# Optimization experiments

Hardware: AMD Instinct MI355X
Metric: run time of the kernel (lower is better)

Reference implementation:

```python
import jax, jax.numpy as jnp
import numpy as np

B, IN, D = 4096, 2048, 2048
NAMES = ["inpgate", "rec_inpgate", "mem_inpgate", "inp", "rec_inp", "readgate",
         "rec_readgate", "mem_readgate", "decoder", "writegate", "rec_writegate",
         "mem_writegate", "encoder"]


def setup_inputs() -> dict:
    key = jax.random.key(0)
    ks = jax.random.split(key, 1 + len(NAMES))
    inp = {
        "x": jax.random.normal(ks[0], (B, IN), jnp.float32),
        "out0": jnp.zeros((B, D), jnp.float32),   # recurrent output state (reset())
        "mem0": jnp.zeros((B, D), jnp.float32),   # memory state (reset())
    }
    for i, n in enumerate(NAMES):
        inp["w_" + n] = jax.random.normal(ks[1 + i], (D, D), jnp.float32) * 0.02
        inp["b_" + n] = jnp.zeros((D,), jnp.float32)
    return inp


def _lin(v, W, b):
    # torch nn.Linear: y = v @ W.T + b, W is [out, in]
    return v @ W.T + b


def reference(x, out0, mem0,
              w_inpgate, b_inpgate, w_rec_inpgate, b_rec_inpgate,
              w_mem_inpgate, b_mem_inpgate, w_inp, b_inp,
              w_rec_inp, b_rec_inp, w_readgate, b_readgate,
              w_rec_readgate, b_rec_readgate, w_mem_readgate, b_mem_readgate,
              w_decoder, b_decoder, w_writegate, b_writegate,
              w_rec_writegate, b_rec_writegate, w_mem_writegate, b_mem_writegate,
              w_encoder, b_encoder):
    sig = jax.nn.sigmoid
    # input block (note: original uses sigmoid here, not tanh)
    block_inp = sig(_lin(x, w_inp, b_inp) + _lin(out0, w_rec_inp, b_rec_inp))
    inp_gate = sig(_lin(x, w_inpgate, b_inpgate)
                   + _lin(mem0, w_mem_inpgate, b_mem_inpgate)
                   + _lin(out0, w_rec_inpgate, b_rec_inpgate))
    read_gate = sig(_lin(x, w_readgate, b_readgate)
                    + _lin(mem0, w_mem_readgate, b_mem_readgate)
                    + _lin(out0, w_rec_readgate, b_rec_readgate))
    decoded_mem = _lin(read_gate * mem0, w_decoder, b_decoder)
    hidden = decoded_mem + block_inp * inp_gate
    write_gate = sig(_lin(x, w_writegate, b_writegate)
                     + _lin(mem0, w_mem_writegate, b_mem_writegate)
                     + _lin(out0, w_rec_writegate, b_rec_writegate))
    enc = jnp.tanh(_lin(hidden, w_encoder, b_encoder))
    mem = (1.0 - write_gate) * mem0 + write_gate * enc
    # torch forward() returns self.out (== hidden_act); mem is internal state
    return hidden
```

## Files before the change

### kernel.cpp

```cpp
#include <hip/hip_runtime.h>
#include <stdint.h>


typedef short bf16x8 __attribute__((ext_vector_type(8)));
typedef float f32x4 __attribute__((ext_vector_type(4)));

#define AS1(p) ((__attribute__((address_space(1))) void*)(uintptr_t)(p))
#define AS3(p) ((__attribute__((address_space(3))) void*)(uint32_t)(uintptr_t)(p))
#define GLD16(gp, lp) __builtin_amdgcn_global_load_lds(AS1(gp), AS3(lp), 16, 0, 0)

__device__ __forceinline__ unsigned short f2bf(float f) {
  union { float f; unsigned u; } c; c.f = f;
  unsigned u = c.u;
  unsigned r = (u + 0x7FFFu + ((u >> 16) & 1u)) >> 16;
  return (unsigned short)r;
}
__device__ __forceinline__ float bf2f(unsigned short h) {
  union { unsigned u; float f; } c; c.u = ((unsigned)h) << 16;
  return c.f;
}
__device__ __forceinline__ float sigf(float x) {
  return 1.0f / (1.0f + __expf(-x));
}

__global__ void init_flags_kernel(int* flags) {
  if (threadIdx.x < 2) flags[threadIdx.x] = 0;
}

struct ConvActArgs {
  const float4* src[3];
  ushort4* dst[3];
  int flagidx[3];
  int n4;
  int* flags;
};

__global__ void conv_acts_kernel(ConvActArgs a) {
  const int arr = blockIdx.y;
  const float4* __restrict__ s = a.src[arr];
  ushort4* __restrict__ d = a.dst[arr];
  unsigned nz = 0;
  for (int i = blockIdx.x * blockDim.x + threadIdx.x; i < a.n4;
       i += gridDim.x * blockDim.x) {
    float4 v = s[i];
    union { float f; unsigned u; } cx, cy, cz, cw;
    cx.f = v.x; cy.f = v.y; cz.f = v.z; cw.f = v.w;
    nz |= cx.u | cy.u | cz.u | cw.u;
    ushort4 o;
    o.x = f2bf(v.x); o.y = f2bf(v.y); o.z = f2bf(v.z); o.w = f2bf(v.w);
    d[i] = o;
  }
  const int fi = a.flagidx[arr];
  if (fi >= 0) {
    if (__any(nz != 0u) && (threadIdx.x & 63) == 0) atomicOr(&a.flags[fi], 1);
  }
}

struct ConvWArgs {
  const float4* src[9];
  ushort4* dst[9];
  int flagidx[9];
  int n4;
  const int* flags;
};

__global__ void conv_weights_kernel(ConvWArgs a) {
  const int arr = blockIdx.y;
  const int fi = a.flagidx[arr];
  if (fi >= 0 && a.flags[fi] == 0) return;
  const float4* __restrict__ s = a.src[arr];
  ushort4* __restrict__ d = a.dst[arr];
  for (int i = blockIdx.x * blockDim.x + threadIdx.x; i < a.n4;
       i += gridDim.x * blockDim.x) {
    float4 v = s[i];
    ushort4 o;
    o.x = f2bf(v.x); o.y = f2bf(v.y); o.z = f2bf(v.z); o.w = f2bf(v.w);
    d[i] = o;
  }
}

struct Job {
  const unsigned short* A0; const unsigned short* W0; const float* b0;
  const unsigned short* A1; const unsigned short* W1; const float* b1;
  const unsigned short* A2; const unsigned short* W2; const float* b2;
  int f0, f1, f2;
  int npairs;
  int jobf;
  const int* flags;
  const float* add;
  float* outF;
  unsigned short* outH;
};

__global__ void __launch_bounds__(256)
gemm_bt_multi(Job j0, Job j1, Job j2) {
  __shared__ __attribute__((aligned(16))) unsigned short sA[128 * 64];
  __shared__ __attribute__((aligned(16))) unsigned short sB[128 * 64];

  const Job jb = (blockIdx.z == 0) ? j0 : ((blockIdx.z == 1) ? j1 : j2);
  if (jb.jobf >= 0 && jb.flags[jb.jobf] == 0) return;

  const int tid = threadIdx.x;
  const int l = tid & 63;
  const int w = tid >> 6;
  const int wm = w >> 1, wn = w & 1;
  const int bm = blockIdx.y, bn = blockIdx.x;

  f32x4 acc[4][4];
#pragma unroll
  for (int i = 0; i < 4; ++i)
#pragma unroll
    for (int j = 0; j < 4; ++j) acc[i][j] = (f32x4){0.f, 0.f, 0.f, 0.f};

  const int srow = l >> 3;
  const int kchS = (l & 7) ^ srow;
  const long long laneA = ((long long)bm * 128 + srow) * 2048 + kchS * 8;
  const long long laneB = ((long long)bn * 128 + srow) * 2048 + kchS * 8;

  auto do_pair = [&](const unsigned short* Ap, const unsigned short* Wp) {
    const unsigned short* ga = Ap + laneA;
    const unsigned short* gb = Wp + laneB;
    for (int kt = 0; kt < 32; ++kt) {
#pragma unroll
      for (int ii = 0; ii < 4; ++ii) {
        const int q = w * 4 + ii;
        GLD16(ga + (long long)(q * 8) * 2048, (char*)sA + q * 1024);
        GLD16(gb + (long long)(q * 8) * 2048, (char*)sB + q * 1024);
      }
      __syncthreads();

#pragma unroll
      for (int ks = 0; ks < 2; ++ks) {
        bf16x8 af[4], bf[4];
        const int c = ks * 4 + (l >> 4);
#pragma unroll
        for (int i = 0; i < 4; ++i) {
          const int ra = wm * 64 + i * 16 + (l & 15);
          const int rb = wn * 64 + i * 16 + (l & 15);
          af[i] = *(const bf16x8*)((const char*)sA +
                  (ra * 128 + ((c ^ (ra & 7)) * 16)));
          bf[i] = *(const bf16x8*)((const char*)sB +
                  (rb * 128 + ((c ^ (rb & 7)) * 16)));
        }
#pragma unroll
        for (int i = 0; i < 4; ++i)
#pragma unroll
          for (int j = 0; j < 4; ++j)
            acc[i][j] = __builtin_amdgcn_mfma_f32_16x16x32_bf16(
                af[i], bf[j], acc[i][j], 0, 0, 0);
      }
      __syncthreads();
      ga += 64;
      gb += 64;
    }
  };

  if (jb.f0 < 0 || jb.flags[jb.f0]) do_pair(jb.A0, jb.W0);
  if (jb.npairs > 1 && (jb.f1 < 0 || jb.flags[jb.f1])) do_pair(jb.A1, jb.W1);
  if (jb.npairs > 2 && (jb.f2 < 0 || jb.flags[jb.f2])) do_pair(jb.A2, jb.W2);

  const int colb = bn * 128 + wn * 64;
  const int rowb = bm * 128 + wm * 64;
#pragma unroll
  for (int j = 0; j < 4; ++j) {
    const int col = colb + j * 16 + (l & 15);
    float bias = 0.f;
    if (jb.b0) bias += jb.b0[col];
    if (jb.npairs > 1 && jb.b1) bias += jb.b1[col];
    if (jb.npairs > 2 && jb.b2) bias += jb.b2[col];
#pragma unroll
    for (int i = 0; i < 4; ++i) {
      const int row0 = rowb + i * 16 + (l >> 4) * 4;
#pragma unroll
      for (int r = 0; r < 4; ++r) {
        const long long idx = (long long)(row0 + r) * 2048 + col;
        float v = acc[i][j][r] + bias;
        if (jb.add) v += jb.add[idx];
        if (jb.outF) jb.outF[idx] = v;
        else jb.outH[idx] = f2bf(v);
      }
    }
  }
}

__global__ void gates_kernel(const ushort4* __restrict__ u1,
                             const ushort4* __restrict__ u2,
                             const ushort4* __restrict__ u3,
                             const float4* __restrict__ mem0,
                             float4* __restrict__ g, ushort4* __restrict__ rg,
                             int n4) {
  int i = blockIdx.x * blockDim.x + threadIdx.x;
  if (i >= n4) return;
  ushort4 a = u1[i], b = u2[i], c = u3[i];
  float4 m = mem0[i];
  float4 go;
  ushort4 ro;
  go.x = sigf(bf2f(a.x)) * sigf(bf2f(b.x)); ro.x = f2bf(sigf(bf2f(c.x)) * m.x);
  go.y = sigf(bf2f(a.y)) * sigf(bf2f(b.y)); ro.y = f2bf(sigf(bf2f(c.y)) * m.y);
  go.z = sigf(bf2f(a.z)) * sigf(bf2f(b.z)); ro.z = f2bf(sigf(bf2f(c.z)) * m.z);
  go.w = sigf(bf2f(a.w)) * sigf(bf2f(b.w)); ro.w = f2bf(sigf(bf2f(c.w)) * m.w);
  g[i] = go;
  rg[i] = ro;
}

extern "C" void kernel_launch(void* const* d_in, const int* in_sizes, int n_in,
                              void* d_out, int out_size, void* d_ws, size_t ws_size,
                              hipStream_t stream) {
  (void)in_sizes; (void)n_in; (void)out_size; (void)ws_size;
  const int Bx = 4096, Dx = 2048;
  const size_t ACT = (size_t)Bx * Dx;
  const size_t WEL = (size_t)Dx * Dx;

  const float* x    = (const float*)d_in[0];
  const float* out0 = (const float*)d_in[1];
  const float* mem0 = (const float*)d_in[2];
  const float* w_inpgate     = (const float*)d_in[3];
  const float* b_inpgate     = (const float*)d_in[4];
  const float* w_rec_inpgate = (const float*)d_in[5];
  const float* b_rec_inpgate = (const float*)d_in[6];
  const float* w_mem_inpgate = (const float*)d_in[7];
  const float* b_mem_inpgate = (const float*)d_in[8];
  const float* w_inp         = (const float*)d_in[9];
  const float* b_inp         = (const float*)d_in[10];
  const float* w_rec_inp     = (const float*)d_in[11];
  const float* b_rec_inp     = (const float*)d_in[12];
  const float* w_readgate    = (const float*)d_in[13];
  const float* b_readgate    = (const float*)d_in[14];
  const float* w_rec_readgate= (const float*)d_in[15];
  const float* b_rec_readgate= (const float*)d_in[16];
  const float* w_mem_readgate= (const float*)d_in[17];
  const float* b_mem_readgate= (const float*)d_in[18];
  const float* w_decoder     = (const float*)d_in[19];
  const float* b_decoder     = (const float*)d_in[20];

  char* ws = (char*)d_ws;
  unsigned short* xb  = (unsigned short*)(ws);
  unsigned short* o0b = xb + ACT;
  unsigned short* m0b = o0b + ACT;
  unsigned short* wb  = m0b + ACT;
  unsigned short* u1 = wb + 9 * WEL;
  unsigned short* u2 = u1 + ACT;
  unsigned short* u3 = u2 + ACT;
  float* g = (float*)(u3 + ACT);
  unsigned short* rg = (unsigned short*)(g + ACT);
  int* flags = (int*)(rg + ACT);

  init_flags_kernel<<<1, 64, 0, stream>>>(flags);

  ConvActArgs aa;
  aa.src[0] = (const float4*)x;    aa.dst[0] = (ushort4*)xb;  aa.flagidx[0] = -1;
  aa.src[1] = (const float4*)out0; aa.dst[1] = (ushort4*)o0b; aa.flagidx[1] = 0;
  aa.src[2] = (const float4*)mem0; aa.dst[2] = (ushort4*)m0b; aa.flagidx[2] = 1;
  aa.n4 = (int)(ACT / 4);
  aa.flags = flags;
  conv_acts_kernel<<<dim3(2048, 3, 1), 256, 0, stream>>>(aa);

  ConvWArgs wa;
  const float* wsrc[9] = {w_inp, w_rec_inp, w_inpgate, w_mem_inpgate,
                          w_rec_inpgate, w_readgate, w_mem_readgate,
                          w_rec_readgate, w_decoder};
  const int wflag[9] = {-1, 0, -1, 1, 0, 1, 1, 0, 1};
  for (int i = 0; i < 9; ++i) {
    wa.src[i] = (const float4*)wsrc[i];
    wa.dst[i] = (ushort4*)(wb + (size_t)i * WEL);
    wa.flagidx[i] = wflag[i];
  }
  wa.n4 = (int)(WEL / 4);
  wa.flags = flags;
  conv_weights_kernel<<<dim3(1024, 9, 1), 256, 0, stream>>>(wa);

  Job J0 = {};
  J0.A0 = xb;  J0.W0 = wb + 0 * WEL; J0.b0 = b_inp;       J0.f0 = -1;
  J0.A1 = o0b; J0.W1 = wb + 1 * WEL; J0.b1 = b_rec_inp;   J0.f1 = 0;
  J0.npairs = 2; J0.jobf = -1; J0.flags = flags; J0.outH = u1;

  Job J1 = {};
  J1.A0 = xb;  J1.W0 = wb + 2 * WEL; J1.b0 = b_inpgate;      J1.f0 = -1;
  J1.A1 = m0b; J1.W1 = wb + 3 * WEL; J1.b1 = b_mem_inpgate;  J1.f1 = 1;
  J1.A2 = o0b; J1.W2 = wb + 4 * WEL; J1.b2 = b_rec_inpgate;  J1.f2 = 0;
  J1.npairs = 3; J1.jobf = -1; J1.flags = flags; J1.outH = u2;

  Job J2 = {};
  J2.A0 = xb;  J2.W0 = wb + 5 * WEL; J2.b0 = b_readgate;      J2.f0 = -1;
  J2.A1 = m0b; J2.W1 = wb + 6 * WEL; J2.b1 = b_mem_readgate;  J2.f1 = 1;
  J2.A2 = o0b; J2.W2 = wb + 7 * WEL; J2.b2 = b_rec_readgate;  J2.f2 = 0;
  J2.npairs = 3; J2.jobf = 1; J2.flags = flags; J2.outH = u3;

  gemm_bt_multi<<<dim3(16, 32, 3), 256, 0, stream>>>(J0, J1, J2);

  gates_kernel<<<(int)(ACT / 4 + 255) / 256, 256, 0, stream>>>(
      (const ushort4*)u1, (const ushort4*)u2, (const ushort4*)u3,
      (const float4*)mem0, (float4*)g, (ushort4*)rg, (int)(ACT / 4));

  Job JD = {};
  JD.A0 = rg; JD.W0 = wb + 8 * WEL; JD.b0 = b_decoder; JD.f0 = 1;
  JD.npairs = 1; JD.jobf = -1; JD.flags = flags;
  JD.add = g; JD.outF = (float*)d_out;
  gemm_bt_multi<<<dim3(16, 32, 1), 256, 0, stream>>>(JD, JD, JD);
}
```

Measured before the change: 425.7 us.

## Fuse input and input-gate GEMMs sharing A tiles, fold gating into epilogue

Adds a dual-output GEMM kernel that loads each activation tile once and multiplies it against two weight matrices, computing the block-input and input-gate preactivations together. When the memory state is flagged zero, the epilogue applies both sigmoids, multiplies them, adds the decoder bias and writes the final output directly. The gates kernel and decoder GEMM then exit early in that case, and the read-gate GEMM already did. This removes a separate pass over the activation tiles, the bf16 intermediate buffers and the elementwise kernel, at the cost of more registers and shared memory per block (two accumulator sets and three LDS tiles), which may lower occupancy.

```diff
diff --git a/kernel.cpp b/kernel.cpp
--- a/kernel.cpp
+++ b/kernel.cpp
@@ -79,6 +79,152 @@
   }
 }
 
+struct DualArgs {
+  const unsigned short *xb, *o0b, *m0b;
+  const unsigned short *Winp, *Wrecinp, *Winpgate, *Wrecinpgate, *Wmeminpgate;
+  const float *b_inp, *b_rec_inp, *b_inpgate, *b_rec_inpgate, *b_mem_inpgate;
+  const float* b_dec;
+  const int* flags;
+  unsigned short *u1, *u2;
+  float* outF;
+};
+
+__global__ void __launch_bounds__(256, 2)
+gemm_dual(DualArgs a) {
+  __shared__ __attribute__((aligned(16))) unsigned short sA[128 * 64];
+  __shared__ __attribute__((aligned(16))) unsigned short sB1[128 * 64];
+  __shared__ __attribute__((aligned(16))) unsigned short sB2[128 * 64];
+
+  const int tid = threadIdx.x;
+  const int l = tid & 63;
+  const int w = tid >> 6;
+  const int wm = w >> 1, wn = w & 1;
+  const int bm = blockIdx.y, bn = blockIdx.x;
+
+  f32x4 acc1[4][4], acc2[4][4];
+#pragma unroll
+  for (int i = 0; i < 4; ++i)
+#pragma unroll
+    for (int j = 0; j < 4; ++j) {
+      acc1[i][j] = (f32x4){0.f, 0.f, 0.f, 0.f};
+      acc2[i][j] = (f32x4){0.f, 0.f, 0.f, 0.f};
+    }
+
+  const int srow = l >> 3;
+  const int kchS = (l & 7) ^ srow;
+  const long long laneA = ((long long)bm * 128 + srow) * 2048 + kchS * 8;
+  const long long laneB = ((long long)bn * 128 + srow) * 2048 + kchS * 8;
+
+  auto do_dual = [&](const unsigned short* Ap, const unsigned short* W1p,
+                     const unsigned short* W2p) {
+    const unsigned short* ga = Ap + laneA;
+    const unsigned short* g1 = W1p + laneB;
+    const unsigned short* g2 = W2p + laneB;
+    for (int kt = 0; kt < 32; ++kt) {
+#pragma unroll
+      for (int ii = 0; ii < 4; ++ii) {
+        const int q = w * 4 + ii;
+        GLD16(ga + (long long)(q * 8) * 2048, (char*)sA + q * 1024);
+        GLD16(g1 + (long long)(q * 8) * 2048, (char*)sB1 + q * 1024);
+        GLD16(g2 + (long long)(q * 8) * 2048, (char*)sB2 + q * 1024);
+      }
+      __syncthreads();
+#pragma unroll
+      for (int ks = 0; ks < 2; ++ks) {
+        bf16x8 af[4], b1[4], b2[4];
+        const int c = ks * 4 + (l >> 4);
+#pragma unroll
+        for (int i = 0; i < 4; ++i) {
+          const int ra = wm * 64 + i * 16 + (l & 15);
+          const int rb = wn * 64 + i * 16 + (l & 15);
+          af[i] = *(const bf16x8*)((const char*)sA + (ra * 128 + ((c ^ (ra & 7)) * 16)));
+          b1[i] = *(const bf16x8*)((const char*)sB1 + (rb * 128 + ((c ^ (rb & 7)) * 16)));
+          b2[i] = *(const bf16x8*)((const char*)sB2 + (rb * 128 + ((c ^ (rb & 7)) * 16)));
+        }
+#pragma unroll
+        for (int i = 0; i < 4; ++i)
+#pragma unroll
+          for (int j = 0; j < 4; ++j) {
+            acc1[i][j] = __builtin_amdgcn_mfma_f32_16x16x32_bf16(
+                af[i], b1[j], acc1[i][j], 0, 0, 0);
+            acc2[i][j] = __builtin_amdgcn_mfma_f32_16x16x32_bf16(
+                af[i], b2[j], acc2[i][j], 0, 0, 0);
+          }
+      }
+      __syncthreads();
+      ga += 64; g1 += 64; g2 += 64;
+    }
+  };
+
+  auto do_single2 = [&](const unsigned short* Ap, const unsigned short* Wp) {
+    const unsigned short* ga = Ap + laneA;
+    const unsigned short* gb = Wp + laneB;
+    for (int kt = 0; kt < 32; ++kt) {
+#pragma unroll
+      for (int ii = 0; ii < 4; ++ii) {
+        const int q = w * 4 + ii;
+        GLD16(ga + (long long)(q * 8) * 2048, (char*)sA + q * 1024);
+        GLD16(gb + (long long)(q * 8) * 2048, (char*)sB2 + q * 1024);
+      }
+      __syncthreads();
+#pragma unroll
+      for (int ks = 0; ks < 2; ++ks) {
+        bf16x8 af[4], b2[4];
+        const int c = ks * 4 + (l >> 4);
+#pragma unroll
+        for (int i = 0; i < 4; ++i) {
+          const int ra = wm * 64 + i * 16 + (l & 15);
+          const int rb = wn * 64 + i * 16 + (l & 15);
+          af[i] = *(const bf16x8*)((const char*)sA + (ra * 128 + ((c ^ (ra & 7)) * 16)));
+          b2[i] = *(const bf16x8*)((const char*)sB2 + (rb * 128 + ((c ^ (rb & 7)) * 16)));
+        }
+#pragma unroll
+        for (int i = 0; i < 4; ++i)
+#pragma unroll
+          for (int j = 0; j < 4; ++j)
+            acc2[i][j] = __builtin_amdgcn_mfma_f32_16x16x32_bf16(
+                af[i], b2[j], acc2[i][j], 0, 0, 0);
+      }
+      __syncthreads();
+      ga += 64; gb += 64;
+    }
+  };
+
+  const int f_out0 = a.flags[0];
+  const int f_mem0 = a.flags[1];
+
+  do_dual(a.xb, a.Winp, a.Winpgate);
+  if (f_out0) do_dual(a.o0b, a.Wrecinp, a.Wrecinpgate);
+  if (f_mem0) do_single2(a.m0b, a.Wmeminpgate);
+
+  const int colb = bn * 128 + wn * 64;
+  const int rowb = bm * 128 + wm * 64;
+  const bool fast = (f_mem0 == 0);
+#pragma unroll
+  for (int j = 0; j < 4; ++j) {
+    const int col = colb + j * 16 + (l & 15);
+    const float s1 = a.b_inp[col] + a.b_rec_inp[col];
+    const float s2 = a.b_inpgate[col] + a.b_rec_inpgate[col] + a.b_mem_inpgate[col];
+    const float bd = fast ? a.b_dec[col] : 0.f;
+#pragma unroll
+    for (int i = 0; i < 4; ++i) {
+      const int row0 = rowb + i * 16 + (l >> 4) * 4;
+#pragma unroll
+      for (int r = 0; r < 4; ++r) {
+        const long long idx = (long long)(row0 + r) * 2048 + col;
+        const float u1v = acc1[i][j][r] + s1;
+        const float u2v = acc2[i][j][r] + s2;
+        if (fast) {
+          a.outF[idx] = sigf(u1v) * sigf(u2v) + bd;
+        } else {
+          a.u1[idx] = f2bf(u1v);
+          a.u2[idx] = f2bf(u2v);
+        }
+      }
+    }
+  }
+}
+
 struct Job {
   const unsigned short* A0; const unsigned short* W0; const float* b0;
   const unsigned short* A1; const unsigned short* W1; const float* b1;
@@ -93,11 +239,10 @@
 };
 
 __global__ void __launch_bounds__(256)
-gemm_bt_multi(Job j0, Job j1, Job j2) {
+gemm_bt_multi(Job jb) {
   __shared__ __attribute__((aligned(16))) unsigned short sA[128 * 64];
   __shared__ __attribute__((aligned(16))) unsigned short sB[128 * 64];
 
-  const Job jb = (blockIdx.z == 0) ? j0 : ((blockIdx.z == 1) ? j1 : j2);
   if (jb.jobf >= 0 && jb.flags[jb.jobf] == 0) return;
 
   const int tid = threadIdx.x;
@@ -128,7 +273,6 @@
         GLD16(gb + (long long)(q * 8) * 2048, (char*)sB + q * 1024);
       }
       __syncthreads();
-
 #pragma unroll
       for (int ks = 0; ks < 2; ++ks) {
         bf16x8 af[4], bf[4];
@@ -137,10 +281,8 @@
         for (int i = 0; i < 4; ++i) {
           const int ra = wm * 64 + i * 16 + (l & 15);
           const int rb = wn * 64 + i * 16 + (l & 15);
-          af[i] = *(const bf16x8*)((const char*)sA +
-                  (ra * 128 + ((c ^ (ra & 7)) * 16)));
-          bf[i] = *(const bf16x8*)((const char*)sB +
-                  (rb * 128 + ((c ^ (rb & 7)) * 16)));
+          af[i] = *(const bf16x8*)((const char*)sA + (ra * 128 + ((c ^ (ra & 7)) * 16)));
+          bf[i] = *(const bf16x8*)((const char*)sB + (rb * 128 + ((c ^ (rb & 7)) * 16)));
         }
 #pragma unroll
         for (int i = 0; i < 4; ++i)
@@ -188,7 +330,8 @@
                              const ushort4* __restrict__ u3,
                              const float4* __restrict__ mem0,
                              float4* __restrict__ g, ushort4* __restrict__ rg,
-                             int n4) {
+                             const int* flags, int n4) {
+  if (flags[1] == 0) return;
   int i = blockIdx.x * blockDim.x + threadIdx.x;
   if (i >= n4) return;
   ushort4 a = u1[i], b = u2[i], c = u3[i];
@@ -269,32 +412,34 @@
   wa.flags = flags;
   conv_weights_kernel<<<dim3(1024, 9, 1), 256, 0, stream>>>(wa);
 
-  Job J0 = {};
-  J0.A0 = xb;  J0.W0 = wb + 0 * WEL; J0.b0 = b_inp;       J0.f0 = -1;
-  J0.A1 = o0b; J0.W1 = wb + 1 * WEL; J0.b1 = b_rec_inp;   J0.f1 = 0;
-  J0.npairs = 2; J0.jobf = -1; J0.flags = flags; J0.outH = u1;
-
-  Job J1 = {};
-  J1.A0 = xb;  J1.W0 = wb + 2 * WEL; J1.b0 = b_inpgate;      J1.f0 = -1;
-  J1.A1 = m0b; J1.W1 = wb + 3 * WEL; J1.b1 = b_mem_inpgate;  J1.f1 = 1;
-  J1.A2 = o0b; J1.W2 = wb + 4 * WEL; J1.b2 = b_rec_inpgate;  J1.f2 = 0;
-  J1.npairs = 3; J1.jobf = -1; J1.flags = flags; J1.outH = u2;
+  DualArgs da;
+  da.xb = xb; da.o0b = o0b; da.m0b = m0b;
+  da.Winp = wb + 0 * WEL;      da.Wrecinp = wb + 1 * WEL;
+  da.Winpgate = wb + 2 * WEL;  da.Wrecinpgate = wb + 4 * WEL;
+  da.Wmeminpgate = wb + 3 * WEL;
+  da.b_inp = b_inp; da.b_rec_inp = b_rec_inp;
+  da.b_inpgate = b_inpgate; da.b_rec_inpgate = b_rec_inpgate;
+  da.b_mem_inpgate = b_mem_inpgate;
+  da.b_dec = b_decoder;
+  da.flags = flags;
+  da.u1 = u1; da.u2 = u2;
+  da.outF = (float*)d_out;
+  gemm_dual<<<dim3(16, 32, 1), 256, 0, stream>>>(da);
 
   Job J2 = {};
   J2.A0 = xb;  J2.W0 = wb + 5 * WEL; J2.b0 = b_readgate;      J2.f0 = -1;
   J2.A1 = m0b; J2.W1 = wb + 6 * WEL; J2.b1 = b_mem_readgate;  J2.f1 = 1;
   J2.A2 = o0b; J2.W2 = wb + 7 * WEL; J2.b2 = b_rec_readgate;  J2.f2 = 0;
   J2.npairs = 3; J2.jobf = 1; J2.flags = flags; J2.outH = u3;
-
-  gemm_bt_multi<<<dim3(16, 32, 3), 256, 0, stream>>>(J0, J1, J2);
+  gemm_bt_multi<<<dim3(16, 32, 1), 256, 0, stream>>>(J2);
 
   gates_kernel<<<(int)(ACT / 4 + 255) / 256, 256, 0, stream>>>(
       (const ushort4*)u1, (const ushort4*)u2, (const ushort4*)u3,
-      (const float4*)mem0, (float4*)g, (ushort4*)rg, (int)(ACT / 4));
+      (const float4*)mem0, (float4*)g, (ushort4*)rg, flags, (int)(ACT / 4));
 
   Job JD = {};
   JD.A0 = rg; JD.W0 = wb + 8 * WEL; JD.b0 = b_decoder; JD.f0 = 1;
-  JD.npairs = 1; JD.jobf = -1; JD.flags = flags;
+  JD.npairs = 1; JD.jobf = 1; JD.flags = flags;
   JD.add = g; JD.outF = (float*)d_out;
-  gemm_bt_multi<<<dim3(16, 32, 1), 256, 0, stream>>>(JD, JD, JD);
-}
+  gemm_bt_multi<<<dim3(16, 32, 1), 256, 0, stream>>>(JD);
+}
```

Result: faster. 367.0 us (-13.8%).
